# Optimization experiments

Measured on AMD Instinct MI355X. Metric: run time of the kernel, lower is better.

The kernel has to match this reference:

```python
import jax, jax.numpy as jnp
import numpy as np

INPUT_SIZE = 1024
HIDDEN_SIZE = 1024
BATCH = 16384


def setup_inputs() -> dict:
    key = jax.random.key(0)
    kx, kh, kw, kb = jax.random.split(key, 4)
    x = jax.random.normal(kx, (BATCH, INPUT_SIZE), dtype=jnp.float32)
    hidden = jax.random.normal(kh, (BATCH, HIDDEN_SIZE), dtype=jnp.float32)
    fan_in = INPUT_SIZE + HIDDEN_SIZE
    bound = 1.0 / np.sqrt(fan_in)
    # torch Linear: weight [out, in], bias [out], uniform(-bound, bound)
    W = jax.random.uniform(kw, (HIDDEN_SIZE, fan_in), minval=-bound, maxval=bound, dtype=jnp.float32)
    b = jax.random.uniform(kb, (HIDDEN_SIZE,), minval=-bound, maxval=bound, dtype=jnp.float32)
    return {"x": x, "hidden": hidden, "W": W, "b": b}


def reference(x, hidden, W, b):
    # Batched equivalent of the per-sample loop: concat features, linear, tanh.
    xh = jnp.concatenate([x, hidden], axis=1)            # [B, in+hid]
    return jnp.tanh(xh @ W.T + b)                        # [B, hid]
```

## Files before the change

kernel.cpp:

```cpp
#include <hip/hip_runtime.h>
#include <hip/hip_bf16.h>


typedef __bf16 bf16_t;
typedef __bf16 bf16x8 __attribute__((ext_vector_type(8)));
typedef float  f32x4  __attribute__((ext_vector_type(4)));

#define M_GLOBAL 16384
#define N_GLOBAL 1024
#define K_GLOBAL 2048
#define IN_STRIDE 1024
#define NT 32

__device__ __forceinline__ float fast_tanh(float v) {
    float e = __expf(2.0f * v);
    return 1.0f - 2.0f * __builtin_amdgcn_rcpf(e + 1.0f);
}

#define XH_UNITS ((long long)M_GLOBAL * K_GLOBAL / 8)
#define W_UNITS  ((long long)N_GLOBAL * K_GLOBAL / 8)

__global__ __launch_bounds__(256)
void cvt_pass(const float* __restrict__ x, const float* __restrict__ h,
              const float* __restrict__ W,
              bf16_t* __restrict__ XHb, bf16_t* __restrict__ Wb)
{
    const long long total = XH_UNITS + W_UNITS;
    for (long long u = (long long)blockIdx.x * 256 + threadIdx.x; u < total;
         u += (long long)gridDim.x * 256) {
        const float* src;
        bf16_t* dst;
        if (u < XH_UNITS) {
            const long long e = u * 8;
            const int row = (int)(e >> 11);
            const int col = (int)(e & 2047);
            src = (col < 1024) ? (x + (long long)row * IN_STRIDE + col)
                               : (h + (long long)row * IN_STRIDE + (col - 1024));
            dst = XHb + e;
        } else {
            const long long e = (u - XH_UNITS) * 8;
            src = W + e;
            dst = Wb + e;
        }
        const float4 v0 = *(const float4*)src;
        const float4 v1 = *(const float4*)(src + 4);
        bf16x8 o;
        o[0] = (bf16_t)v0.x; o[1] = (bf16_t)v0.y;
        o[2] = (bf16_t)v0.z; o[3] = (bf16_t)v0.w;
        o[4] = (bf16_t)v1.x; o[5] = (bf16_t)v1.y;
        o[6] = (bf16_t)v1.z; o[7] = (bf16_t)v1.w;
        *(bf16x8*)dst = o;
    }
}

__device__ __forceinline__ void gload_lds16(const bf16_t* g, bf16_t* l) {
    __builtin_amdgcn_global_load_lds(
        (const __attribute__((address_space(1))) void*)g,
        (__attribute__((address_space(3))) void*)l, 16, 0, 0);
}

__global__ __launch_bounds__(1024)
void gemm_w16(const bf16_t* __restrict__ XHb, const bf16_t* __restrict__ Wb,
              const float* __restrict__ bias, float* __restrict__ out)
{
    __shared__ __align__(16) bf16_t lds[2 * 32768];

    const int tid = threadIdx.x;
    const int x = blockIdx.x & 7;
    const int g = blockIdx.x >> 3;
    const int bm = (x * 8 + (g & 7)) * 256;
    const int bn = (g >> 3) * 256;

    const int lane = tid & 63;
    const int wid  = tid >> 6;
    const int wm = wid >> 2;
    const int wn = wid & 3;
    const int lr = lane & 15;
    const int lk = lane >> 4;
    const int s7 = lr & 7;

    const int srow = lane >> 3;
    const int scol = ((lane & 7) ^ srow) * 8;
    const bf16_t* aS = XHb + (size_t)(bm + wid * 8 + srow) * K_GLOBAL + scol;
    const bf16_t* bS = Wb  + (size_t)(bn + wid * 8 + srow) * K_GLOBAL + scol;

    const int aRd = (wm >> 1) * 8192 + ((wm & 1) * 64 + lr) * 64;
    const int bRd = (2 + (wn >> 1)) * 8192 + ((wn & 1) * 64 + lr) * 64;

    f32x4 acc[4][4];
#pragma unroll
    for (int i = 0; i < 4; ++i)
#pragma unroll
        for (int j = 0; j < 4; ++j)
            acc[i][j] = (f32x4){0.f, 0.f, 0.f, 0.f};

#define STAGE_FULL(T, D) {                                                    \
    _Pragma("unroll")                                                         \
    for (int p_ = 0; p_ < 4; ++p_) {                                          \
        const bf16_t* g_ = ((p_ < 2) ? aS : bS)                               \
            + (size_t)((p_ & 1) * 128) * K_GLOBAL + (T) * 64;                 \
        gload_lds16(g_, lds + (D) * 32768 + p_ * 8192 + wid * 512);           \
    }                                                                         \
}

#define BAR() { asm volatile("" ::: "memory");                                \
                __builtin_amdgcn_s_barrier();                                 \
                asm volatile("" ::: "memory"); }
#define VM0() asm volatile("s_waitcnt vmcnt(0)" ::: "memory")

    STAGE_FULL(0, 0);
    VM0();
    BAR();

    for (int t = 0; t < NT; ++t) {
        const int dbo = (t & 1) * 32768;

        if (t + 1 < NT) STAGE_FULL(t + 1, (t + 1) & 1);

        __builtin_amdgcn_s_setprio(1);
#pragma unroll
        for (int kk = 0; kk < 2; ++kk) {
            const int sl = ((kk * 4 + lk) ^ s7) * 8;
            bf16x8 bq[4];
#pragma unroll
            for (int nf = 0; nf < 4; ++nf)
                bq[nf] = *(const bf16x8*)(lds + dbo + bRd + nf * 1024 + sl);
#pragma unroll
            for (int mf = 0; mf < 4; ++mf) {
                bf16x8 af = *(const bf16x8*)(lds + dbo + aRd + mf * 1024 + sl);
#pragma unroll
                for (int nf = 0; nf < 4; ++nf)
                    acc[mf][nf] = __builtin_amdgcn_mfma_f32_16x16x32_bf16(
                        af, bq[nf], acc[mf][nf], 0, 0, 0);
            }
        }
        __builtin_amdgcn_s_setprio(0);

        if (t + 1 < NT) { VM0(); BAR(); }
    }

#undef STAGE_FULL
#undef BAR
#undef VM0

    float bv[4];
#pragma unroll
    for (int nf = 0; nf < 4; ++nf)
        bv[nf] = bias[bn + wn * 64 + nf * 16 + lr];
#pragma unroll
    for (int mf = 0; mf < 4; ++mf) {
#pragma unroll
        for (int nf = 0; nf < 4; ++nf) {
            const int col = bn + wn * 64 + nf * 16 + lr;
#pragma unroll
            for (int r = 0; r < 4; ++r) {
                const int row = bm + wm * 64 + mf * 16 + lk * 4 + r;
                out[(size_t)row * N_GLOBAL + col] = fast_tanh(acc[mf][nf][r] + bv[nf]);
            }
        }
    }
}

#define FNT 32
__global__ __launch_bounds__(256, 2)
void rnncell_fused(const float* __restrict__ x, const float* __restrict__ h,
                   const float* __restrict__ W, const float* __restrict__ bias,
                   float* __restrict__ out)
{
    __shared__ __align__(16) bf16_t As[2][128 * 64];
    __shared__ __align__(16) bf16_t Bs[2][128 * 64];

    const int tid = threadIdx.x;
    const int bid = blockIdx.x;
    const int bm = (bid >> 3) * 128;
    const int bn = (bid & 7) * 128;

    const int lane = tid & 63;
    const int wid  = tid >> 6;
    const int wr = (wid >> 1) * 64;
    const int wc = (wid & 1) * 64;
    const int lr = lane & 15;
    const int lk = lane >> 4;

    const int row0 = tid >> 3;
    const int sl0  = tid & 7;

    f32x4 acc[4][4];
#pragma unroll
    for (int i = 0; i < 4; ++i)
#pragma unroll
        for (int j = 0; j < 4; ++j)
            acc[i][j] = (f32x4){0.f, 0.f, 0.f, 0.f};

    float4 la[4][2], lb[4][2];

#define F_LOAD_A(T) do {                                                      \
    const int k0_ = (T) * 64;                                                 \
    const float* sA_ = (k0_ < 1024)                                           \
        ? (x + (size_t)bm * IN_STRIDE + k0_)                                  \
        : (h + (size_t)bm * IN_STRIDE + (k0_ - 1024));                        \
    _Pragma("unroll")                                                         \
    for (int i_ = 0; i_ < 4; ++i_) {                                          \
        const float* pa_ = sA_ + (size_t)(row0 + i_ * 32) * IN_STRIDE + sl0 * 8; \
        la[i_][0] = *(const float4*)(pa_);                                    \
        la[i_][1] = *(const float4*)(pa_ + 4);                                \
    }                                                                         \
} while (0)

#define F_LOAD_B(T) do {                                                      \
    const float* sB_ = W + (size_t)bn * K_GLOBAL + (T) * 64;                  \
    _Pragma("unroll")                                                         \
    for (int i_ = 0; i_ < 4; ++i_) {                                          \
        const float* pb_ = sB_ + (size_t)(row0 + i_ * 32) * K_GLOBAL + sl0 * 8; \
        lb[i_][0] = *(const float4*)(pb_);                                    \
        lb[i_][1] = *(const float4*)(pb_ + 4);                                \
    }                                                                         \
} while (0)

    F_LOAD_A(0);
    F_LOAD_B(0);

    for (int t = 0; t < FNT; ++t) {
        bf16_t* __restrict__ Ab = As[t & 1];
        bf16_t* __restrict__ Bb = Bs[t & 1];

#pragma unroll
        for (int i = 0; i < 4; ++i) {
            const int row = row0 + i * 32;
            const int ssl = sl0 ^ (row & 7);
            bf16x8 va;
            va[0] = (bf16_t)la[i][0].x; va[1] = (bf16_t)la[i][0].y;
            va[2] = (bf16_t)la[i][0].z; va[3] = (bf16_t)la[i][0].w;
            va[4] = (bf16_t)la[i][1].x; va[5] = (bf16_t)la[i][1].y;
            va[6] = (bf16_t)la[i][1].z; va[7] = (bf16_t)la[i][1].w;
            *(bf16x8*)(Ab + row * 64 + ssl * 8) = va;
        }
#pragma unroll
        for (int i = 0; i < 4; ++i) {
            const int row = row0 + i * 32;
            const int ssl = sl0 ^ (row & 7);
            bf16x8 vb;
            vb[0] = (bf16_t)lb[i][0].x; vb[1] = (bf16_t)lb[i][0].y;
            vb[2] = (bf16_t)lb[i][0].z; vb[3] = (bf16_t)lb[i][0].w;
            vb[4] = (bf16_t)lb[i][1].x; vb[5] = (bf16_t)lb[i][1].y;
            vb[6] = (bf16_t)lb[i][1].z; vb[7] = (bf16_t)lb[i][1].w;
            *(bf16x8*)(Bb + row * 64 + ssl * 8) = vb;
        }

        __syncthreads();

        if (t + 1 < FNT) F_LOAD_A(t + 1);

#pragma unroll
        for (int kk = 0; kk < 2; ++kk) {
            bf16x8 af[4], bfr[4];
#pragma unroll
            for (int mf = 0; mf < 4; ++mf) {
                const int row = wr + mf * 16 + lr;
                const int sl  = (kk * 4 + lk) ^ (row & 7);
                af[mf] = *(const bf16x8*)(Ab + row * 64 + sl * 8);
            }
#pragma unroll
            for (int nf = 0; nf < 4; ++nf) {
                const int row = wc + nf * 16 + lr;
                const int sl  = (kk * 4 + lk) ^ (row & 7);
                bfr[nf] = *(const bf16x8*)(Bb + row * 64 + sl * 8);
            }
#pragma unroll
            for (int mf = 0; mf < 4; ++mf)
#pragma unroll
                for (int nf = 0; nf < 4; ++nf)
                    acc[mf][nf] = __builtin_amdgcn_mfma_f32_16x16x32_bf16(
                        af[mf], bfr[nf], acc[mf][nf], 0, 0, 0);
        }

        if (t + 1 < FNT) F_LOAD_B(t + 1);
    }
#undef F_LOAD_A
#undef F_LOAD_B

    float bv[4];
#pragma unroll
    for (int nf = 0; nf < 4; ++nf)
        bv[nf] = bias[bn + wc + nf * 16 + lr];
#pragma unroll
    for (int mf = 0; mf < 4; ++mf) {
#pragma unroll
        for (int nf = 0; nf < 4; ++nf) {
            const int col = bn + wc + nf * 16 + lr;
#pragma unroll
            for (int r = 0; r < 4; ++r) {
                const int row = bm + wr + mf * 16 + lk * 4 + r;
                out[(size_t)row * N_GLOBAL + col] = fast_tanh(acc[mf][nf][r] + bv[nf]);
            }
        }
    }
}

extern "C" void kernel_launch(void* const* d_in, const int* in_sizes, int n_in,
                              void* d_out, int out_size, void* d_ws, size_t ws_size,
                              hipStream_t stream) {
    (void)in_sizes; (void)n_in; (void)out_size;
    const float* x = (const float*)d_in[0];
    const float* h = (const float*)d_in[1];
    const float* W = (const float*)d_in[2];
    const float* b = (const float*)d_in[3];
    float* out = (float*)d_out;

    const size_t need = ((size_t)M_GLOBAL + N_GLOBAL) * K_GLOBAL * sizeof(bf16_t);
    if (ws_size >= need) {
        bf16_t* XHb = (bf16_t*)d_ws;
        bf16_t* Wb  = XHb + (size_t)M_GLOBAL * K_GLOBAL;
        cvt_pass<<<2048, 256, 0, stream>>>(x, h, W, XHb, Wb);
        gemm_w16<<<256, 1024, 0, stream>>>(XHb, Wb, b, out);
    } else {
        rnncell_fused<<<1024, 256, 0, stream>>>(x, h, W, b, out);
    }
}
```

Baseline: 99.35 us.

## Fuse fp32-to-bf16 activation conversion into GEMM A-tile loading

Removes the separate pre-pass that converted x and h to bf16 in workspace; only W is still pre-converted. The GEMM now loads fp32 activations into registers, converts them to bf16 and writes them swizzled into LDS, while B still uses direct global-to-LDS loads. This avoids writing and re-reading a 64MB bf16 activation buffer. In exchange, each block reads twice the bytes of A, and the conversion and LDS stores add latency to the double-buffer step.

Measured after the change: 85.36 us, median of 2. -14.1%, faster.

```diff
diff --git a/kernel.cpp b/kernel.cpp
--- a/kernel.cpp
+++ b/kernel.cpp
@@ -17,39 +17,22 @@
     return 1.0f - 2.0f * __builtin_amdgcn_rcpf(e + 1.0f);
 }
 
-#define XH_UNITS ((long long)M_GLOBAL * K_GLOBAL / 8)
-#define W_UNITS  ((long long)N_GLOBAL * K_GLOBAL / 8)
+#define W_UNITS ((long long)N_GLOBAL * K_GLOBAL / 8)
 
 __global__ __launch_bounds__(256)
-void cvt_pass(const float* __restrict__ x, const float* __restrict__ h,
-              const float* __restrict__ W,
-              bf16_t* __restrict__ XHb, bf16_t* __restrict__ Wb)
+void cvt_w(const float* __restrict__ W, bf16_t* __restrict__ Wb)
 {
-    const long long total = XH_UNITS + W_UNITS;
-    for (long long u = (long long)blockIdx.x * 256 + threadIdx.x; u < total;
+    for (long long u = (long long)blockIdx.x * 256 + threadIdx.x; u < W_UNITS;
          u += (long long)gridDim.x * 256) {
-        const float* src;
-        bf16_t* dst;
-        if (u < XH_UNITS) {
-            const long long e = u * 8;
-            const int row = (int)(e >> 11);
-            const int col = (int)(e & 2047);
-            src = (col < 1024) ? (x + (long long)row * IN_STRIDE + col)
-                               : (h + (long long)row * IN_STRIDE + (col - 1024));
-            dst = XHb + e;
-        } else {
-            const long long e = (u - XH_UNITS) * 8;
-            src = W + e;
-            dst = Wb + e;
-        }
-        const float4 v0 = *(const float4*)src;
-        const float4 v1 = *(const float4*)(src + 4);
+        const long long e = u * 8;
+        const float4 v0 = *(const float4*)(W + e);
+        const float4 v1 = *(const float4*)(W + e + 4);
         bf16x8 o;
         o[0] = (bf16_t)v0.x; o[1] = (bf16_t)v0.y;
         o[2] = (bf16_t)v0.z; o[3] = (bf16_t)v0.w;
         o[4] = (bf16_t)v1.x; o[5] = (bf16_t)v1.y;
         o[6] = (bf16_t)v1.z; o[7] = (bf16_t)v1.w;
-        *(bf16x8*)dst = o;
+        *(bf16x8*)(Wb + e) = o;
     }
 }
 
@@ -60,16 +43,17 @@
 }
 
 __global__ __launch_bounds__(1024)
-void gemm_w16(const bf16_t* __restrict__ XHb, const bf16_t* __restrict__ Wb,
-              const float* __restrict__ bias, float* __restrict__ out)
+void gemm_fa(const float* __restrict__ x, const float* __restrict__ h,
+             const bf16_t* __restrict__ Wb,
+             const float* __restrict__ bias, float* __restrict__ out)
 {
     __shared__ __align__(16) bf16_t lds[2 * 32768];
 
     const int tid = threadIdx.x;
-    const int x = blockIdx.x & 7;
-    const int g = blockIdx.x >> 3;
-    const int bm = (x * 8 + (g & 7)) * 256;
-    const int bn = (g >> 3) * 256;
+    const int xx = blockIdx.x & 7;
+    const int gg = blockIdx.x >> 3;
+    const int bm = (xx * 8 + (gg & 7)) * 256;
+    const int bn = (gg >> 3) * 256;
 
     const int lane = tid & 63;
     const int wid  = tid >> 6;
@@ -80,9 +64,13 @@
     const int s7 = lr & 7;
 
     const int srow = lane >> 3;
-    const int scol = ((lane & 7) ^ srow) * 8;
-    const bf16_t* aS = XHb + (size_t)(bm + wid * 8 + srow) * K_GLOBAL + scol;
-    const bf16_t* bS = Wb  + (size_t)(bn + wid * 8 + srow) * K_GLOBAL + scol;
+    const int q8   = lane & 7;
+
+    const int arow0 = bm + wid * 8 + srow;
+    const bf16_t* bS = Wb + (size_t)(bn + wid * 8 + srow) * K_GLOBAL
+                          + (q8 ^ srow) * 8;
+
+    const int aWr = wid * 512 + srow * 64 + (q8 ^ srow) * 8;
 
     const int aRd = (wm >> 1) * 8192 + ((wm & 1) * 64 + lr) * 64;
     const int bRd = (2 + (wn >> 1)) * 8192 + ((wn & 1) * 64 + lr) * 64;
@@ -94,28 +82,56 @@
         for (int j = 0; j < 4; ++j)
             acc[i][j] = (f32x4){0.f, 0.f, 0.f, 0.f};
 
-#define STAGE_FULL(T, D) {                                                    \
-    _Pragma("unroll")                                                         \
-    for (int p_ = 0; p_ < 4; ++p_) {                                          \
-        const bf16_t* g_ = ((p_ < 2) ? aS : bS)                               \
-            + (size_t)((p_ & 1) * 128) * K_GLOBAL + (T) * 64;                 \
-        gload_lds16(g_, lds + (D) * 32768 + p_ * 8192 + wid * 512);           \
+    float4 ar[2][2];
+
+#define LOAD_A(T) {                                                           \
+    const int k0_ = (T) * 64;                                                 \
+    const float* s_ = (k0_ < 1024) ? (x + k0_) : (h + (k0_ - 1024));          \
+    _Pragma("unroll")                                                         \
+    for (int p_ = 0; p_ < 2; ++p_) {                                          \
+        const float* r_ = s_ + (size_t)(arow0 + p_ * 128) * IN_STRIDE + q8 * 8; \
+        ar[p_][0] = *(const float4*)(r_);                                     \
+        ar[p_][1] = *(const float4*)(r_ + 4);                                 \
+    }                                                                         \
+}
+
+#define CVT_WRITE_A(D) {                                                      \
+    _Pragma("unroll")                                                         \
+    for (int p_ = 0; p_ < 2; ++p_) {                                          \
+        bf16x8 v_;                                                            \
+        v_[0] = (bf16_t)ar[p_][0].x; v_[1] = (bf16_t)ar[p_][0].y;             \
+        v_[2] = (bf16_t)ar[p_][0].z; v_[3] = (bf16_t)ar[p_][0].w;             \
+        v_[4] = (bf16_t)ar[p_][1].x; v_[5] = (bf16_t)ar[p_][1].y;             \
+        v_[6] = (bf16_t)ar[p_][1].z; v_[7] = (bf16_t)ar[p_][1].w;             \
+        *(bf16x8*)(lds + (D) * 32768 + p_ * 8192 + aWr) = v_;                 \
+    }                                                                         \
+}
+
+#define STAGE_B(T, D) {                                                       \
+    _Pragma("unroll")                                                         \
+    for (int p_ = 2; p_ < 4; ++p_) {                                          \
+        gload_lds16(bS + (size_t)((p_ & 1) * 128) * K_GLOBAL + (T) * 64,      \
+                    lds + (D) * 32768 + p_ * 8192 + wid * 512);               \
     }                                                                         \
 }
 
 #define BAR() { asm volatile("" ::: "memory");                                \
                 __builtin_amdgcn_s_barrier();                                 \
                 asm volatile("" ::: "memory"); }
-#define VM0() asm volatile("s_waitcnt vmcnt(0)" ::: "memory")
-
-    STAGE_FULL(0, 0);
+#define VM0()   asm volatile("s_waitcnt vmcnt(0)" ::: "memory")
+#define LGKM0() asm volatile("s_waitcnt lgkmcnt(0)" ::: "memory")
+
+    LOAD_A(0);
+    STAGE_B(0, 0);
     VM0();
+    CVT_WRITE_A(0);
+    LGKM0();
     BAR();
 
     for (int t = 0; t < NT; ++t) {
-        const int dbo = (t & 1) * 32768;
-
-        if (t + 1 < NT) STAGE_FULL(t + 1, (t + 1) & 1);
+        const bf16_t* lb = lds + (t & 1) * 32768;
+
+        if (t + 1 < NT) { LOAD_A(t + 1); STAGE_B(t + 1, (t + 1) & 1); }
 
         __builtin_amdgcn_s_setprio(1);
 #pragma unroll
@@ -124,10 +140,10 @@
             bf16x8 bq[4];
 #pragma unroll
             for (int nf = 0; nf < 4; ++nf)
-                bq[nf] = *(const bf16x8*)(lds + dbo + bRd + nf * 1024 + sl);
+                bq[nf] = *(const bf16x8*)(lb + bRd + nf * 1024 + sl);
 #pragma unroll
             for (int mf = 0; mf < 4; ++mf) {
-                bf16x8 af = *(const bf16x8*)(lds + dbo + aRd + mf * 1024 + sl);
+                bf16x8 af = *(const bf16x8*)(lb + aRd + mf * 1024 + sl);
 #pragma unroll
                 for (int nf = 0; nf < 4; ++nf)
                     acc[mf][nf] = __builtin_amdgcn_mfma_f32_16x16x32_bf16(
@@ -136,12 +152,20 @@
         }
         __builtin_amdgcn_s_setprio(0);
 
-        if (t + 1 < NT) { VM0(); BAR(); }
-    }
-
-#undef STAGE_FULL
+        if (t + 1 < NT) {
+            VM0();
+            CVT_WRITE_A((t + 1) & 1);
+            LGKM0();
+            BAR();
+        }
+    }
+
+#undef LOAD_A
+#undef CVT_WRITE_A
+#undef STAGE_B
 #undef BAR
 #undef VM0
+#undef LGKM0
 
     float bv[4];
 #pragma unroll
@@ -307,12 +331,11 @@
     const float* b = (const float*)d_in[3];
     float* out = (float*)d_out;
 
-    const size_t need = ((size_t)M_GLOBAL + N_GLOBAL) * K_GLOBAL * sizeof(bf16_t);
+    const size_t need = (size_t)N_GLOBAL * K_GLOBAL * sizeof(bf16_t);
     if (ws_size >= need) {
-        bf16_t* XHb = (bf16_t*)d_ws;
-        bf16_t* Wb  = XHb + (size_t)M_GLOBAL * K_GLOBAL;
-        cvt_pass<<<2048, 256, 0, stream>>>(x, h, W, XHb, Wb);
-        gemm_w16<<<256, 1024, 0, stream>>>(XHb, Wb, b, out);
+        bf16_t* Wb = (bf16_t*)d_ws;
+        cvt_w<<<512, 256, 0, stream>>>(W, Wb);
+        gemm_fa<<<256, 1024, 0, stream>>>(x, h, Wb, b, out);
     } else {
         rnncell_fused<<<1024, 256, 0, stream>>>(x, h, W, b, out);
     }
```
